# Performance work log

Hardware: AMD Instinct MI355X
Metric: run time of the kernel (lower is better)

The kernel has to match this reference:

```python
import jax, jax.numpy as jnp
import numpy as np

BN_EPS = 1e-5

def setup_inputs() -> dict:
    key = jax.random.key(0)
    k1, k2 = jax.random.split(key)
    B, C, H, W = 16, 256, 128, 128
    x = jax.random.normal(k1, (B, C, H, W), dtype=jnp.float32)
    w = jax.random.normal(k2, (C, 3), dtype=jnp.float32) * 0.1  # depthwise conv1d weight [c,1,3] squeezed
    gamma = jnp.ones((C,), dtype=jnp.float32)
    beta = jnp.zeros((C,), dtype=jnp.float32)
    running_mean = jnp.zeros((C,), dtype=jnp.float32)
    running_var = jnp.ones((C,), dtype=jnp.float32)
    return {"x": x, "w": w, "gamma": gamma, "beta": beta,
            "running_mean": running_mean, "running_var": running_var}


def reference(x, w, gamma, beta, running_mean, running_var):
    b, c, h, wd = x.shape
    xf = x.reshape(b, c, h * wd)
    mean = xf.mean(-1)                      # AdaptiveAvgPool2d(1)  -> [b,c]
    mx = xf.max(-1)                         # AdaptiveMaxPool2d(1)  -> [b,c]
    std = jnp.std(xf, axis=-1, ddof=1)      # torch std, unbiased   -> [b,c]
    u = jnp.stack([mean, mx, std], axis=-1)  # [b,c,3]
    # MS: per-batch median over the full [c,3] slice, then cube the deviation
    med = jnp.median(u.reshape(b, -1), axis=-1)  # [b]
    u = (u - med[:, None, None]) ** 3
    # depthwise Conv1d(k=3, groups=c) on length-3 input -> length-1 output
    z = jnp.einsum('bck,ck->bc', u, w)
    # BatchNorm1d (eval mode)
    z = (z - running_mean) * jax.lax.rsqrt(running_var + BN_EPS) * gamma + beta
    g = jax.nn.sigmoid(z)                    # [b,c]
    return x * g[:, :, None, None]
```

## Files before the change

kernel.cpp:

```cpp
#include <hip/hip_runtime.h>
#include <math.h>


typedef float fvec4 __attribute__((ext_vector_type(4)));

__global__ __launch_bounds__(256) void stats_kernel(
        const float* __restrict__ x, float* __restrict__ u, int HW) {
    const int bc  = blockIdx.x;
    const int tid = threadIdx.x;
    const float4* __restrict__ x4 =
        (const float4*)(x + (size_t)bc * (size_t)HW);
    const int n4 = HW >> 2;

    float s0 = 0.f, q0 = 0.f, m0 = -INFINITY;
    float s1 = 0.f, q1 = 0.f, m1 = -INFINITY;
    float s2 = 0.f, q2 = 0.f, m2 = -INFINITY;
    float s3 = 0.f, q3 = 0.f, m3 = -INFINITY;

    if (n4 == 4096) {
        #pragma unroll
        for (int half = 0; half < 2; ++half) {
            float4 r[8];
            const int bi = tid + half * 2048;
            #pragma unroll
            for (int k = 0; k < 8; ++k) r[k] = x4[bi + k * 256];
            #pragma unroll
            for (int k = 0; k < 8; k += 4) {
                float4 a = r[k], b = r[k + 1], c = r[k + 2], d = r[k + 3];
                s0 += (a.x + a.y) + (a.z + a.w);
                q0 += (a.x * a.x + a.y * a.y) + (a.z * a.z + a.w * a.w);
                m0 = fmaxf(m0, fmaxf(fmaxf(a.x, a.y), fmaxf(a.z, a.w)));
                s1 += (b.x + b.y) + (b.z + b.w);
                q1 += (b.x * b.x + b.y * b.y) + (b.z * b.z + b.w * b.w);
                m1 = fmaxf(m1, fmaxf(fmaxf(b.x, b.y), fmaxf(b.z, b.w)));
                s2 += (c.x + c.y) + (c.z + c.w);
                q2 += (c.x * c.x + c.y * c.y) + (c.z * c.z + c.w * c.w);
                m2 = fmaxf(m2, fmaxf(fmaxf(c.x, c.y), fmaxf(c.z, c.w)));
                s3 += (d.x + d.y) + (d.z + d.w);
                q3 += (d.x * d.x + d.y * d.y) + (d.z * d.z + d.w * d.w);
                m3 = fmaxf(m3, fmaxf(fmaxf(d.x, d.y), fmaxf(d.z, d.w)));
            }
        }
    } else {
        for (int i = tid; i < n4; i += 256) {
            float4 a = x4[i];
            s0 += (a.x + a.y) + (a.z + a.w);
            q0 += (a.x * a.x + a.y * a.y) + (a.z * a.z + a.w * a.w);
            m0 = fmaxf(m0, fmaxf(fmaxf(a.x, a.y), fmaxf(a.z, a.w)));
        }
    }
    float s = (s0 + s1) + (s2 + s3);
    float q = (q0 + q1) + (q2 + q3);
    float mx = fmaxf(fmaxf(m0, m1), fmaxf(m2, m3));

    for (int off = 32; off > 0; off >>= 1) {
        s  += __shfl_down(s, off);
        q  += __shfl_down(q, off);
        mx  = fmaxf(mx, __shfl_down(mx, off));
    }
    __shared__ float ss[4], sq[4], sm[4];
    const int wid = tid >> 6, lane = tid & 63;
    if (lane == 0) { ss[wid] = s; sq[wid] = q; sm[wid] = mx; }
    __syncthreads();
    if (tid == 0) {
        float S = ss[0] + ss[1] + ss[2] + ss[3];
        float Q = sq[0] + sq[1] + sq[2] + sq[3];
        float M = fmaxf(fmaxf(sm[0], sm[1]), fmaxf(sm[2], sm[3]));
        float mean = S / (float)HW;
        float var  = (Q - S * mean) / (float)(HW - 1);
        var = fmaxf(var, 0.f);
        float* up = u + (size_t)bc * 3;
        up[0] = mean;
        up[1] = M;
        up[2] = sqrtf(var);
    }
}

__global__ void median_gate_kernel(const float* __restrict__ u,
                                   const float* __restrict__ w,
                                   const float* __restrict__ gamma,
                                   const float* __restrict__ beta,
                                   const float* __restrict__ rmean,
                                   const float* __restrict__ rvar,
                                   float* __restrict__ g, int C) {
    const int b   = blockIdx.x;
    const int tid = threadIdx.x;
    const int NV  = C * 3;
    __shared__ float sv[768];
    __shared__ float ma, mb;

    const float* ub = u + (size_t)b * NV;
    for (int i = tid; i < NV; i += 256) sv[i] = ub[i];
    __syncthreads();

    float v0 = sv[tid], v1 = sv[tid + 256], v2 = sv[tid + 512];
    int lt0 = 0, eq0 = 0, lt1 = 0, eq1 = 0, lt2 = 0, eq2 = 0;
    for (int i = 0; i < NV; ++i) {
        float o = sv[i];
        lt0 += (o < v0); eq0 += (o == v0);
        lt1 += (o < v1); eq1 += (o == v1);
        lt2 += (o < v2); eq2 += (o == v2);
    }
    const int r0 = (NV - 1) / 2;
    const int r1 = NV / 2;
    if (lt0 <= r0 && r0 < lt0 + eq0) ma = v0;
    if (lt1 <= r0 && r0 < lt1 + eq1) ma = v1;
    if (lt2 <= r0 && r0 < lt2 + eq2) ma = v2;
    if (lt0 <= r1 && r1 < lt0 + eq0) mb = v0;
    if (lt1 <= r1 && r1 < lt1 + eq1) mb = v1;
    if (lt2 <= r1 && r1 < lt2 + eq2) mb = v2;
    __syncthreads();

    const float med = 0.5f * (ma + mb);
    if (tid < C) {
        const int c = tid;
        float z = 0.f;
        #pragma unroll
        for (int k = 0; k < 3; ++k) {
            float d = sv[c * 3 + k] - med;
            z += (d * d * d) * w[c * 3 + k];
        }
        z = (z - rmean[c]) * rsqrtf(rvar[c] + 1e-5f) * gamma[c] + beta[c];
        g[(size_t)b * C + c] = 1.f / (1.f + expf(-z));
    }
}

__global__ __launch_bounds__(256) void scale_kernel(
        const float* __restrict__ x, const float* __restrict__ g,
        float* __restrict__ out, int HW) {
    const int bc = blockIdx.x;
    const float gv = g[bc];
    const size_t base = (size_t)bc * (size_t)HW;
    const fvec4* __restrict__ x4 = (const fvec4*)(x + base);
    fvec4* __restrict__ o4 = (fvec4*)(out + base);
    const int n4 = HW >> 2;
    if (n4 == 4096) {
        #pragma unroll
        for (int half = 0; half < 2; ++half) {
            const int bi = (int)threadIdx.x + half * 2048;
            fvec4 r[8];
            #pragma unroll
            for (int k = 0; k < 8; ++k)
                r[k] = x4[bi + k * 256];
            #pragma unroll
            for (int k = 0; k < 8; ++k)
                __builtin_nontemporal_store(r[k] * gv, &o4[bi + k * 256]);
        }
    } else {
        for (int i = threadIdx.x; i < n4; i += 256) {
            fvec4 v = x4[i];
            __builtin_nontemporal_store(v * gv, &o4[i]);
        }
    }
}

extern "C" void kernel_launch(void* const* d_in, const int* in_sizes, int n_in,
                              void* d_out, int out_size, void* d_ws, size_t ws_size,
                              hipStream_t stream) {
    const float* x     = (const float*)d_in[0];
    const float* w     = (const float*)d_in[1];
    const float* gamma = (const float*)d_in[2];
    const float* beta  = (const float*)d_in[3];
    const float* rmean = (const float*)d_in[4];
    const float* rvar  = (const float*)d_in[5];
    float* out = (float*)d_out;

    const int C  = in_sizes[2];
    const int B  = 16;
    const int HW = in_sizes[0] / (B * C);

    float* u = (float*)d_ws;
    float* g = u + (size_t)B * C * 3;

    stats_kernel<<<B * C, 256, 0, stream>>>(x, u, HW);
    median_gate_kernel<<<B, 256, 0, stream>>>(u, w, gamma, beta, rmean, rvar, g, C);
    scale_kernel<<<B * C, 256, 0, stream>>>(x, g, out, HW);
}
```

Measured before the change: 159.8 us.

## Fuse median/gate computation into scale kernel, recomputing median per block

Merges the per-batch median and gate kernel into the scaling kernel, so each (b,c) block reloads the batch's stats, recomputes the median and its own gate, then scales. The x loads are issued up front so the median compute can overlap memory latency. This removes a low-parallelism 16-block kernel and one launch. In exchange it adds redundant O(C·3) median work per block and higher register use from the 16-entry load buffer.

```diff
diff --git a/kernel.cpp b/kernel.cpp
--- a/kernel.cpp
+++ b/kernel.cpp
@@ -76,44 +76,55 @@
     }
 }
 
-__global__ void median_gate_kernel(const float* __restrict__ u,
-                                   const float* __restrict__ w,
-                                   const float* __restrict__ gamma,
-                                   const float* __restrict__ beta,
-                                   const float* __restrict__ rmean,
-                                   const float* __restrict__ rvar,
-                                   float* __restrict__ g, int C) {
-    const int b   = blockIdx.x;
+__global__ __launch_bounds__(256, 4) void gate_scale_kernel(
+        const float* __restrict__ x,
+        const float* __restrict__ u,
+        const float* __restrict__ w,
+        const float* __restrict__ gamma,
+        const float* __restrict__ beta,
+        const float* __restrict__ rmean,
+        const float* __restrict__ rvar,
+        float* __restrict__ out, int HW, int C) {
+    const int bc  = blockIdx.x;
+    const int b   = bc / C;
+    const int c   = bc - b * C;
     const int tid = threadIdx.x;
     const int NV  = C * 3;
+    const size_t base = (size_t)bc * (size_t)HW;
+    const fvec4* __restrict__ x4 = (const fvec4*)(x + base);
+    fvec4* __restrict__ o4 = (fvec4*)(out + base);
+    const int n4 = HW >> 2;
+
     __shared__ float sv[768];
     __shared__ float ma, mb;
 
-    const float* ub = u + (size_t)b * NV;
-    for (int i = tid; i < NV; i += 256) sv[i] = ub[i];
-    __syncthreads();
+    if (n4 == 4096) {
+        fvec4 r[16];
+        #pragma unroll
+        for (int k = 0; k < 16; ++k) r[k] = x4[tid + k * 256];
 
-    float v0 = sv[tid], v1 = sv[tid + 256], v2 = sv[tid + 512];
-    int lt0 = 0, eq0 = 0, lt1 = 0, eq1 = 0, lt2 = 0, eq2 = 0;
-    for (int i = 0; i < NV; ++i) {
-        float o = sv[i];
-        lt0 += (o < v0); eq0 += (o == v0);
-        lt1 += (o < v1); eq1 += (o == v1);
-        lt2 += (o < v2); eq2 += (o == v2);
-    }
-    const int r0 = (NV - 1) / 2;
-    const int r1 = NV / 2;
-    if (lt0 <= r0 && r0 < lt0 + eq0) ma = v0;
-    if (lt1 <= r0 && r0 < lt1 + eq1) ma = v1;
-    if (lt2 <= r0 && r0 < lt2 + eq2) ma = v2;
-    if (lt0 <= r1 && r1 < lt0 + eq0) mb = v0;
-    if (lt1 <= r1 && r1 < lt1 + eq1) mb = v1;
-    if (lt2 <= r1 && r1 < lt2 + eq2) mb = v2;
-    __syncthreads();
+        const float* ub = u + (size_t)b * NV;
+        for (int i = tid; i < NV; i += 256) sv[i] = ub[i];
+        __syncthreads();
+        float v0 = sv[tid], v1 = sv[tid + 256], v2 = sv[tid + 512];
+        int lt0 = 0, eq0 = 0, lt1 = 0, eq1 = 0, lt2 = 0, eq2 = 0;
+        for (int i = 0; i < NV; ++i) {
+            float o = sv[i];
+            lt0 += (o < v0); eq0 += (o == v0);
+            lt1 += (o < v1); eq1 += (o == v1);
+            lt2 += (o < v2); eq2 += (o == v2);
+        }
+        const int r0 = (NV - 1) / 2;
+        const int r1 = NV / 2;
+        if (lt0 <= r0 && r0 < lt0 + eq0) ma = v0;
+        if (lt1 <= r0 && r0 < lt1 + eq1) ma = v1;
+        if (lt2 <= r0 && r0 < lt2 + eq2) ma = v2;
+        if (lt0 <= r1 && r1 < lt0 + eq0) mb = v0;
+        if (lt1 <= r1 && r1 < lt1 + eq1) mb = v1;
+        if (lt2 <= r1 && r1 < lt2 + eq2) mb = v2;
+        __syncthreads();
+        const float med = 0.5f * (ma + mb);
 
-    const float med = 0.5f * (ma + mb);
-    if (tid < C) {
-        const int c = tid;
         float z = 0.f;
         #pragma unroll
         for (int k = 0; k < 3; ++k) {
@@ -121,33 +132,42 @@
             z += (d * d * d) * w[c * 3 + k];
         }
         z = (z - rmean[c]) * rsqrtf(rvar[c] + 1e-5f) * gamma[c] + beta[c];
-        g[(size_t)b * C + c] = 1.f / (1.f + expf(-z));
-    }
-}
+        const float gv = 1.f / (1.f + expf(-z));
 
-__global__ __launch_bounds__(256) void scale_kernel(
-        const float* __restrict__ x, const float* __restrict__ g,
-        float* __restrict__ out, int HW) {
-    const int bc = blockIdx.x;
-    const float gv = g[bc];
-    const size_t base = (size_t)bc * (size_t)HW;
-    const fvec4* __restrict__ x4 = (const fvec4*)(x + base);
-    fvec4* __restrict__ o4 = (fvec4*)(out + base);
-    const int n4 = HW >> 2;
-    if (n4 == 4096) {
         #pragma unroll
-        for (int half = 0; half < 2; ++half) {
-            const int bi = (int)threadIdx.x + half * 2048;
-            fvec4 r[8];
-            #pragma unroll
-            for (int k = 0; k < 8; ++k)
-                r[k] = x4[bi + k * 256];
-            #pragma unroll
-            for (int k = 0; k < 8; ++k)
-                __builtin_nontemporal_store(r[k] * gv, &o4[bi + k * 256]);
+        for (int k = 0; k < 16; ++k)
+            __builtin_nontemporal_store(r[k] * gv, &o4[tid + k * 256]);
+    } else {
+        const float* ub = u + (size_t)b * NV;
+        for (int i = tid; i < NV; i += 256) sv[i] = ub[i];
+        __syncthreads();
+        float v0 = sv[tid], v1 = sv[tid + 256], v2 = sv[tid + 512];
+        int lt0 = 0, eq0 = 0, lt1 = 0, eq1 = 0, lt2 = 0, eq2 = 0;
+        for (int i = 0; i < NV; ++i) {
+            float o = sv[i];
+            lt0 += (o < v0); eq0 += (o == v0);
+            lt1 += (o < v1); eq1 += (o == v1);
+            lt2 += (o < v2); eq2 += (o == v2);
         }
-    } else {
-        for (int i = threadIdx.x; i < n4; i += 256) {
+        const int r0 = (NV - 1) / 2;
+        const int r1 = NV / 2;
+        if (lt0 <= r0 && r0 < lt0 + eq0) ma = v0;
+        if (lt1 <= r0 && r0 < lt1 + eq1) ma = v1;
+        if (lt2 <= r0 && r0 < lt2 + eq2) ma = v2;
+        if (lt0 <= r1 && r1 < lt0 + eq0) mb = v0;
+        if (lt1 <= r1 && r1 < lt1 + eq1) mb = v1;
+        if (lt2 <= r1 && r1 < lt2 + eq2) mb = v2;
+        __syncthreads();
+        const float med = 0.5f * (ma + mb);
+        float z = 0.f;
+        #pragma unroll
+        for (int k = 0; k < 3; ++k) {
+            float d = sv[c * 3 + k] - med;
+            z += (d * d * d) * w[c * 3 + k];
+        }
+        z = (z - rmean[c]) * rsqrtf(rvar[c] + 1e-5f) * gamma[c] + beta[c];
+        const float gv = 1.f / (1.f + expf(-z));
+        for (int i = tid; i < n4; i += 256) {
             fvec4 v = x4[i];
             __builtin_nontemporal_store(v * gv, &o4[i]);
         }
@@ -170,9 +190,8 @@
     const int HW = in_sizes[0] / (B * C);
 
     float* u = (float*)d_ws;
-    float* g = u + (size_t)B * C * 3;
 
     stats_kernel<<<B * C, 256, 0, stream>>>(x, u, HW);
-    median_gate_kernel<<<B, 256, 0, stream>>>(u, w, gamma, beta, rmean, rvar, g, C);
-    scale_kernel<<<B * C, 256, 0, stream>>>(x, g, out, HW);
+    gate_scale_kernel<<<B * C, 256, 0, stream>>>(x, u, w, gamma, beta, rmean,
+                                                 rvar, out, HW, C);
 }
```

Result: slower. 316.3 us (+98.0%).

## Stream scale kernel input through LDS with double-buffered async global loads

Applied to the files above, without the earlier changes.

Rewrites the scale kernel to pull each 1024-float4 chunk into shared memory with direct global-to-LDS loads, double-buffered so the next chunk loads while the current one is scaled and stored. The aim is to keep more loads in flight and overlap load latency with the nontemporal stores, instead of issuing eight register loads per half. In exchange it adds 32KB of LDS per block, which may lower occupancy, plus a barrier per chunk and hand-written waitcnt values that must match the hardware counter semantics.

```diff
diff --git a/kernel.cpp b/kernel.cpp
--- a/kernel.cpp
+++ b/kernel.cpp
@@ -128,26 +128,55 @@
 __global__ __launch_bounds__(256) void scale_kernel(
         const float* __restrict__ x, const float* __restrict__ g,
         float* __restrict__ out, int HW) {
-    const int bc = blockIdx.x;
+    const int bc  = blockIdx.x;
+    const int tid = threadIdx.x;
     const float gv = g[bc];
     const size_t base = (size_t)bc * (size_t)HW;
     const fvec4* __restrict__ x4 = (const fvec4*)(x + base);
     fvec4* __restrict__ o4 = (fvec4*)(out + base);
     const int n4 = HW >> 2;
-    if (n4 == 4096) {
+
+    if ((n4 & 1023) == 0) {
+        __shared__ fvec4 sbuf[2][1024];
+        const int w    = tid >> 6;
+        const int lane = tid & 63;
+        const int nch  = n4 >> 10;
+
         #pragma unroll
-        for (int half = 0; half < 2; ++half) {
-            const int bi = (int)threadIdx.x + half * 2048;
-            fvec4 r[8];
+        for (int j = 0; j < 4; ++j) {
+            const int seg = j * 4 + w;
+            __builtin_amdgcn_global_load_lds(
+                (const __attribute__((address_space(1))) void*)&x4[seg * 64 + lane],
+                (__attribute__((address_space(3))) void*)&sbuf[0][seg * 64],
+                16, 0, 0);
+        }
+        for (int c = 0; c < nch; ++c) {
+            const int cur = c & 1;
+            if (c + 1 < nch) {
+                #pragma unroll
+                for (int j = 0; j < 4; ++j) {
+                    const int seg = j * 4 + w;
+                    __builtin_amdgcn_global_load_lds(
+                        (const __attribute__((address_space(1))) void*)
+                            &x4[(c + 1) * 1024 + seg * 64 + lane],
+                        (__attribute__((address_space(3))) void*)
+                            &sbuf[cur ^ 1][seg * 64],
+                        16, 0, 0);
+                }
+                asm volatile("s_waitcnt vmcnt(4)" ::: "memory");
+            } else {
+                asm volatile("s_waitcnt vmcnt(0)" ::: "memory");
+            }
+            __builtin_amdgcn_s_barrier();
             #pragma unroll
-            for (int k = 0; k < 8; ++k)
-                r[k] = x4[bi + k * 256];
-            #pragma unroll
-            for (int k = 0; k < 8; ++k)
-                __builtin_nontemporal_store(r[k] * gv, &o4[bi + k * 256]);
+            for (int j = 0; j < 4; ++j) {
+                fvec4 v = sbuf[cur][tid + j * 256];
+                __builtin_nontemporal_store(v * gv, &o4[c * 1024 + j * 256 + tid]);
+            }
+            __builtin_amdgcn_s_barrier();
         }
     } else {
-        for (int i = threadIdx.x; i < n4; i += 256) {
+        for (int i = tid; i < n4; i += 256) {
             fvec4 v = x4[i];
             __builtin_nontemporal_store(v * gv, &o4[i]);
         }
```

New measurement: 161.2 us. Within noise of the previous version (+0.9%).
